# Performance work log

Hardware: AMD Instinct MI355X
Metric: run time of the kernel (lower is better)

The kernel has to match this reference:

```python
import jax, jax.numpy as jnp
import numpy as np

B, S, E, D, H, DH, FF, L = 8, 1024, 256, 1024, 16, 64, 4096, 12
TIME_DIM = 4096
MAX_PERIOD = 10000.0


def setup_inputs() -> dict:
    key = jax.random.key(0)
    ks = jax.random.split(key, 12)
    n = lambda k, shp: jax.random.normal(k, shp, dtype=jnp.float32) * 0.02
    return dict(
        inputs=jax.random.normal(ks[0], (B, S, 2 * E), dtype=jnp.float32),
        time=jax.random.uniform(ks[1], (B,), dtype=jnp.float32),
        in_W=n(ks[2], (2 * E, D)), in_b=jnp.zeros((D,), jnp.float32),
        out_W=n(ks[3], (D, E)), out_b=jnp.zeros((E,), jnp.float32),
        t_W1=n(ks[4], (D, TIME_DIM)), t_b1=jnp.zeros((TIME_DIM,), jnp.float32),
        t_W2=n(ks[5], (TIME_DIM, D)), t_b2=jnp.zeros((D,), jnp.float32),
        ln_scale=jnp.ones((L, D), jnp.float32),
        ln_bias=jnp.zeros((L, D), jnp.float32),
        proj_W=n(ks[6], (L, D, 3 * H * DH + 2 * FF)),
        attn_W=n(ks[7], (L, H * DH, D)),
        ff_W=n(ks[8], (L, FF, D)),
    )


def _layernorm(x, g, b):
    m = jnp.mean(x, axis=-1, keepdims=True)
    v = jnp.mean(jnp.square(x - m), axis=-1, keepdims=True)
    return (x - m) * jax.lax.rsqrt(v + 1e-5) * g + b


def reference(inputs, time, in_W, in_b, out_W, out_b, t_W1, t_b1, t_W2, t_b2,
              ln_scale, ln_bias, proj_W, attn_W, ff_W):
    # --- time embedding (SinusoidalTimeEmbedding -> Linear -> GELU -> Linear -> GELU) ---
    half = D // 2
    inv_ts = jnp.exp(jnp.arange(half, dtype=jnp.float32) * (-np.log(MAX_PERIOD) / (half - 1.0)))
    ts = time[:, None] * inv_ts[None, :]                      # [B, D/2]
    temb = jnp.concatenate([jnp.sin(ts), jnp.cos(ts)], -1)     # [B, D]
    temb = jax.nn.gelu(temb @ t_W1 + t_b1, approximate=False)
    temb = jax.nn.gelu(temb @ t_W2 + t_b2, approximate=False)  # [B, D]
    # --- fixed position embedding ---
    inv_freq = 1.0 / (MAX_PERIOD ** (jnp.arange(0, D, 2, dtype=jnp.float32) / D))
    sinu = jnp.arange(S, dtype=jnp.float32)[:, None] * inv_freq[None, :]  # [S, D/2]
    pos = jnp.concatenate([jnp.sin(sinu), jnp.cos(sinu)], -1)             # [S, D]
    # --- input projection + additive embeddings ---
    h = inputs @ in_W + in_b + pos[None] + temb[:, None, :]    # [B, S, D]
    scale = 1.0 / np.sqrt(DH)

    def block(h, params):
        g, bln, Wp, Wa, Wf = params
        u = _layernorm(h, g, bln)
        proj = u @ Wp                                          # [B, S, 3*H*DH + 2*FF]
        q, k, v, ff, gate = jnp.split(
            proj, [H * DH, 2 * H * DH, 3 * H * DH, 3 * H * DH + FF], axis=-1)
        q = q.reshape(B, S, H, DH).transpose(0, 2, 1, 3)       # [B, H, S, DH]
        k = k.reshape(B, S, H, DH).transpose(0, 2, 1, 3)
        v = v.reshape(B, S, H, DH).transpose(0, 2, 1, 3)
        score = jnp.einsum('bhsd,bhtd->bhst', q, k) * scale
        w = jax.nn.softmax(score, axis=-1)
        a = jnp.einsum('bhst,bhtd->bhsd', w, v)
        a = a.transpose(0, 2, 1, 3).reshape(B, S, H * DH)      # merge heads
        attn_out = a @ Wa
        ff_out = (ff * jax.nn.gelu(gate, approximate=True)) @ Wf  # tanh GELU per torch
        return h + attn_out + ff_out, None

    h, _ = jax.lax.scan(block, h, (ln_scale, ln_bias, proj_W, attn_W, ff_W))
    return h @ out_W + out_b
```

## Files before the change

### kernel.cpp

```cpp
#include <hip/hip_runtime.h>
#include <hip/hip_bf16.h>
#include <math.h>

static constexpr int B_ = 8, S_ = 1024, E_ = 256, D_ = 1024, H_ = 16, DH_ = 64,
                     FF_ = 4096, L_ = 12, TDIM_ = 4096;
static constexpr int BS_ = B_ * S_;
static constexpr int PROJN_ = 3 * H_ * DH_ + 2 * FF_;
static constexpr int PROJ3_ = 3 * H_ * DH_;
static constexpr int AOW_ = H_ * DH_ + FF_;

typedef __attribute__((ext_vector_type(8))) short bf16x8;
typedef __attribute__((ext_vector_type(4))) short bf16x4;
typedef __attribute__((ext_vector_type(4))) float f32x4;

__device__ __forceinline__ float b2f(short b) {
    return __uint_as_float(((unsigned)(unsigned short)b) << 16);
}
__device__ __forceinline__ short f2b(float f) {
    __hip_bfloat16 h = __float2bfloat16(f);
    return *reinterpret_cast<short*>(&h);
}
__device__ __forceinline__ float gelu_exact(float x) {
    return 0.5f * x * (1.f + erff(x * 0.70710678118654752440f));
}
__device__ __forceinline__ float gelu_tanh(float x) {
    float u2 = 1.59576912160573070f * (x + 0.044715f * x * x * x);
    return x / (1.f + __expf(-u2));
}

#define GLOAD16(g, l)                                                     \
    __builtin_amdgcn_global_load_lds(                                     \
        (const __attribute__((address_space(1))) void*)(g),               \
        (__attribute__((address_space(3))) void*)(l), 16, 0, 0)

__global__ void temb0_kernel(const float* __restrict__ time, float* __restrict__ temb0) {
    int b = blockIdx.x;
    int i = threadIdx.x;
    float inv_ts = expf((float)i * (-logf(10000.f) / 511.f));
    float ts = time[b] * inv_ts;
    temb0[b * D_ + i] = sinf(ts);
    temb0[b * D_ + 512 + i] = cosf(ts);
}

__global__ void pos_kernel(float* __restrict__ pos) {
    int s = blockIdx.x;
    int j = threadIdx.x;
    float inv_freq = expf((float)j * (-logf(10000.f) / 512.f));
    float arg = (float)s * inv_freq;
    pos[s * D_ + j] = sinf(arg);
    pos[s * D_ + 512 + j] = cosf(arg);
}

__global__ void tmlp_kernel(const float* __restrict__ A, const float* __restrict__ Bw,
                            const float* __restrict__ bias, float* __restrict__ C,
                            int K, int N) {
    __shared__ float Ast[8][256];
    __shared__ float red2[16][16][9];
    int t = threadIdx.x;
    int col = t & 15, ks = t >> 4;
    int n = blockIdx.x * 16 + col;
    float acc[8];
#pragma unroll
    for (int b = 0; b < 8; ++b) acc[b] = 0.f;
    for (int c0 = 0; c0 < K; c0 += 256) {
#pragma unroll
        for (int i = 0; i < 8; ++i) {
            int idx = t + i * 256;
            Ast[idx >> 8][idx & 255] = A[(idx >> 8) * K + c0 + (idx & 255)];
        }
        __syncthreads();
#pragma unroll
        for (int i = 0; i < 16; ++i) {
            int k = ks * 16 + i;
            float w = Bw[(size_t)(c0 + k) * N + n];
#pragma unroll
            for (int b = 0; b < 8; ++b) acc[b] = fmaf(Ast[b][k], w, acc[b]);
        }
        __syncthreads();
    }
#pragma unroll
    for (int b = 0; b < 8; ++b) red2[ks][col][b] = acc[b];
    __syncthreads();
    if (t < 128) {
        int c2 = t >> 3, b = t & 7;
        float s = 0.f;
#pragma unroll
        for (int k2 = 0; k2 < 16; ++k2) s += red2[k2][c2][b];
        int nn = blockIdx.x * 16 + c2;
        C[(size_t)b * N + nn] = gelu_exact(s + bias[nn]);
    }
}

__global__ void addpe_kernel(float* __restrict__ h, const float* __restrict__ pos,
                             const float* __restrict__ temb) {
    size_t idx = (size_t)blockIdx.x * 256 + threadIdx.x;
    int d = (int)(idx & 1023);
    int s = (int)((idx >> 10) & 1023);
    int b = (int)(idx >> 20);
    h[idx] += pos[s * D_ + d] + temb[b * D_ + d];
}

__global__ void f2b4_kernel(const float* __restrict__ in, __hip_bfloat16* __restrict__ out) {
    size_t i = ((size_t)blockIdx.x * 256 + threadIdx.x) * 4;
    float4 v = *reinterpret_cast<const float4*>(in + i);
    bf16x4 o;
    o[0] = f2b(v.x); o[1] = f2b(v.y); o[2] = f2b(v.z); o[3] = f2b(v.w);
    *reinterpret_cast<bf16x4*>(reinterpret_cast<short*>(out) + i) = o;
}

template <int PERM>
__global__ void convT_kernel(const float* __restrict__ W, __hip_bfloat16* __restrict__ Wt,
                             int K, int N, int outStride, int colOff) {
    __shared__ float tile[64][65];
    int t = threadIdx.x;
    int n0 = blockIdx.x * 64, k0 = blockIdx.y * 64;
#pragma unroll
    for (int i = 0; i < 4; ++i) {
        int idx = t + i * 256;
        int row = idx >> 4, c4 = (idx & 15) * 4;
        float4 v = *reinterpret_cast<const float4*>(W + (size_t)(k0 + row) * N + n0 + c4);
        tile[row][c4 + 0] = v.x; tile[row][c4 + 1] = v.y;
        tile[row][c4 + 2] = v.z; tile[row][c4 + 3] = v.w;
    }
    __syncthreads();
#pragma unroll
    for (int i = 0; i < 4; ++i) {
        int idx = t + i * 256;
        int n = idx >> 4, k4 = (idx & 15) * 4;
        int ng = n0 + n;
        size_t orow;
        if (PERM) {
            if (ng < 3072) orow = ng;
            else if (ng < 7168) { int j = ng - 3072; orow = 3072 + (j >> 7) * 256 + (j & 127); }
            else { int j = ng - 7168; orow = 3072 + (j >> 7) * 256 + 128 + (j & 127); }
        } else {
            orow = ng;
        }
        bf16x4 o;
#pragma unroll
        for (int j = 0; j < 4; ++j) o[j] = f2b(tile[k4 + j][n]);
        *reinterpret_cast<bf16x4*>(reinterpret_cast<short*>(Wt) + orow * outStride + colOff + k0 + k4) = o;
    }
}

__global__ void ln_kernel(const float* __restrict__ h, const float* __restrict__ g,
                          const float* __restrict__ bb, __hip_bfloat16* __restrict__ u) {
    int row = blockIdx.x;
    int t = threadIdx.x;
    const float4 v = reinterpret_cast<const float4*>(h + (size_t)row * D_)[t];
    __shared__ float red[8];
    float s = v.x + v.y + v.z + v.w;
    for (int m8 = 1; m8 < 64; m8 <<= 1) s += __shfl_xor(s, m8, 64);
    if ((t & 63) == 0) red[t >> 6] = s;
    __syncthreads();
    float mean = (red[0] + red[1] + red[2] + red[3]) * (1.f / 1024.f);
    float dx = v.x - mean, dy = v.y - mean, dz = v.z - mean, dw = v.w - mean;
    float sq = dx * dx + dy * dy + dz * dz + dw * dw;
    for (int m8 = 1; m8 < 64; m8 <<= 1) sq += __shfl_xor(sq, m8, 64);
    if ((t & 63) == 0) red[4 + (t >> 6)] = sq;
    __syncthreads();
    float var = (red[4] + red[5] + red[6] + red[7]) * (1.f / 1024.f);
    float inv = rsqrtf(var + 1e-5f);
    int c = t * 4;
    bf16x4 o;
    o[0] = f2b(dx * inv * g[c + 0] + bb[c + 0]);
    o[1] = f2b(dy * inv * g[c + 1] + bb[c + 1]);
    o[2] = f2b(dz * inv * g[c + 2] + bb[c + 2]);
    o[3] = f2b(dw * inv * g[c + 3] + bb[c + 3]);
    *reinterpret_cast<bf16x4*>(reinterpret_cast<short*>(u) + (size_t)row * D_ + c) = o;
}

template <int MODE, int BIAS>
__global__ __launch_bounds__(256) void mfma_gemm(
    const __hip_bfloat16* __restrict__ A, const __hip_bfloat16* __restrict__ Bt,
    const float* __restrict__ bias, float* __restrict__ Cf,
    __hip_bfloat16* __restrict__ Cb, int M, int N, int K) {
    __shared__ __align__(16) char As[128 * 64];
    __shared__ __align__(16) char Bs[128 * 64];
    int t = threadIdx.x;
    int lane = t & 63, wid = t >> 6;
    int m0 = blockIdx.y * 128, n0 = blockIdx.x * 128;
    size_t rowb = (size_t)K * 2;
    int srow = wid * 32 + (lane >> 2);
    int scol = (lane & 3) * 16;
    const char* ag0 = (const char*)A + (size_t)(m0 + srow) * rowb + scol;
    const char* ag1 = (const char*)A + (size_t)(m0 + srow + 16) * rowb + scol;
    const char* bg0 = (const char*)Bt + (size_t)(n0 + srow) * rowb + scol;
    const char* bg1 = (const char*)Bt + (size_t)(n0 + srow + 16) * rowb + scol;
    int lb0 = wid * 32 * 64;
    int lb1 = lb0 + 16 * 64;
    int wr = (wid >> 1) * 64, wc = (wid & 1) * 64;
    int lr = lane & 15;
    int a_base = (wr + lr) * 64 + (lane >> 4) * 16;
    int b_base = (wc + lr) * 64 + (lane >> 4) * 16;
    f32x4 acc[4][4] = {};
    int nkt = K >> 5;
    for (int kt = 0; kt < nkt; ++kt) {
        GLOAD16(ag0, As + lb0);
        GLOAD16(ag1, As + lb1);
        GLOAD16(bg0, Bs + lb0);
        GLOAD16(bg1, Bs + lb1);
        ag0 += 64; ag1 += 64; bg0 += 64; bg1 += 64;
        __syncthreads();
        bf16x8 af[4], bf[4];
#pragma unroll
        for (int f = 0; f < 4; ++f) {
            af[f] = *reinterpret_cast<const bf16x8*>(As + a_base + f * 1024);
            bf[f] = *reinterpret_cast<const bf16x8*>(Bs + b_base + f * 1024);
        }
        __builtin_amdgcn_s_setprio(1);
#pragma unroll
        for (int i = 0; i < 4; ++i)
#pragma unroll
            for (int j = 0; j < 4; ++j)
                acc[i][j] = __builtin_amdgcn_mfma_f32_16x16x32_bf16(af[i], bf[j], acc[i][j], 0, 0, 0);
        __builtin_amdgcn_s_setprio(0);
        __syncthreads();
    }
    int crow0 = m0 + wr + (lane >> 4) * 4;
    int ccol0 = n0 + wc + lr;
#pragma unroll
    for (int i = 0; i < 4; ++i) {
#pragma unroll
        for (int j = 0; j < 4; ++j) {
            int col = ccol0 + j * 16;
            float bv = BIAS ? bias[col] : 0.f;
            f32x4 v = acc[i][j];
#pragma unroll
            for (int r = 0; r < 4; ++r) {
                size_t o = (size_t)(crow0 + i * 16 + r) * N + col;
                float val = v[r] + bv;
                if (MODE == 0) Cf[o] = val;
                else if (MODE == 1) Cb[o] = __float2bfloat16(val);
                else Cf[o] += val;
            }
        }
    }
}

template <int MODE>
__global__ __launch_bounds__(512, 2) void gemm256(
    const __hip_bfloat16* __restrict__ A, const __hip_bfloat16* __restrict__ Bt,
    float* __restrict__ Cf, __hip_bfloat16* __restrict__ Cb,
    __hip_bfloat16* __restrict__ Fb, int M, int N, int K) {
    __shared__ __align__(16) char lds[131072];
    const int t = threadIdx.x;
    const int lane = t & 63, wid = t >> 6;
    const int lr = lane & 15, g = lane >> 4;
    const int wr = wid >> 2, wc = wid & 3;
    const int m0 = blockIdx.y * 256, n0 = blockIdx.x * 256;
    const size_t rowb = (size_t)K * 2;
    const int NT = K >> 6;
    const int srow = lane >> 2;
    const int scol = ((lane & 3) ^ (((lane >> 5) & 1) << 1)) * 16;
    const int ga = (g ^ (((lr >> 3) & 1) << 1)) * 16;
    const int arow = wr * 16 + lr;
    const int brow = wc * 16 + lr;
    const char* Ab = (const char*)A;
    const char* Bb = (const char*)Bt;

    auto stage = [&](int mat, int kt, int hh) {
        if (kt >= NT) return;
        int rbase = (mat ? n0 : m0) + hh * 128 + wid * 16 + srow;
        const char* src = (mat ? Bb : Ab) + (size_t)rbase * rowb + (size_t)kt * 128 + scol;
        char* dst = lds + mat * 65536 + (kt & 1) * 32768 + (hh * 128 + wid * 16) * 64;
        GLOAD16(src, dst);
        GLOAD16(src + 64, dst + 16384);
    };

    f32x4 acc[8][4] = {};
    bf16x8 af[4][2], bfr[4][2];

    stage(0, 0, 0); stage(0, 0, 1); stage(1, 0, 0); stage(1, 0, 1);
    stage(0, 1, 0); stage(1, 1, 0); stage(1, 1, 1);
    asm volatile("s_waitcnt vmcnt(6)" ::: "memory");
    __builtin_amdgcn_s_barrier();

    for (int kt = 0; kt < NT; ++kt) {
        const int p = kt & 1;
        const char* la = lds + p * 32768;
        const char* lb = lds + 65536 + p * 32768;
#pragma unroll
        for (int mi = 0; mi < 4; ++mi)
#pragma unroll
            for (int kk = 0; kk < 2; ++kk)
                af[mi][kk] = *reinterpret_cast<const bf16x8*>(
                    la + kk * 16384 + (mi * 32 + arow) * 64 + ga);
#pragma unroll
        for (int n = 0; n < 2; ++n)
#pragma unroll
            for (int kk = 0; kk < 2; ++kk)
                bfr[n][kk] = *reinterpret_cast<const bf16x8*>(
                    lb + kk * 16384 + (n * 64 + brow) * 64 + ga);
        stage(0, kt + 1, 1);
        __builtin_amdgcn_s_barrier();
        asm volatile("s_waitcnt lgkmcnt(0)" ::: "memory");
        __builtin_amdgcn_sched_barrier(0);
        __builtin_amdgcn_s_setprio(1);
#pragma unroll
        for (int mi = 0; mi < 4; ++mi)
#pragma unroll
            for (int n = 0; n < 2; ++n)
#pragma unroll
                for (int kk = 0; kk < 2; ++kk)
                    acc[mi][n] = __builtin_amdgcn_mfma_f32_16x16x32_bf16(
                        af[mi][kk], bfr[n][kk], acc[mi][n], 0, 0, 0);
        __builtin_amdgcn_s_setprio(0);
        __builtin_amdgcn_s_barrier();
#pragma unroll
        for (int n = 2; n < 4; ++n)
#pragma unroll
            for (int kk = 0; kk < 2; ++kk)
                bfr[n][kk] = *reinterpret_cast<const bf16x8*>(
                    lb + kk * 16384 + (n * 64 + brow) * 64 + ga);
        stage(0, kt + 2, 0);
        __builtin_amdgcn_s_barrier();
        asm volatile("s_waitcnt lgkmcnt(0)" ::: "memory");
        __builtin_amdgcn_sched_barrier(0);
        __builtin_amdgcn_s_setprio(1);
#pragma unroll
        for (int mi = 0; mi < 4; ++mi)
#pragma unroll
            for (int n = 2; n < 4; ++n)
#pragma unroll
                for (int kk = 0; kk < 2; ++kk)
                    acc[mi][n] = __builtin_amdgcn_mfma_f32_16x16x32_bf16(
                        af[mi][kk], bfr[n][kk], acc[mi][n], 0, 0, 0);
        __builtin_amdgcn_s_setprio(0);
        __builtin_amdgcn_s_barrier();
#pragma unroll
        for (int mi = 0; mi < 4; ++mi)
#pragma unroll
            for (int kk = 0; kk < 2; ++kk)
                af[mi][kk] = *reinterpret_cast<const bf16x8*>(
                    la + kk * 16384 + ((mi + 4) * 32 + arow) * 64 + ga);
        stage(1, kt + 2, 0);
        __builtin_amdgcn_s_barrier();
        asm volatile("s_waitcnt lgkmcnt(0)" ::: "memory");
        __builtin_amdgcn_sched_barrier(0);
        __builtin_amdgcn_s_setprio(1);
#pragma unroll
        for (int mi = 0; mi < 4; ++mi)
#pragma unroll
            for (int n = 2; n < 4; ++n)
#pragma unroll
                for (int kk = 0; kk < 2; ++kk)
                    acc[mi + 4][n] = __builtin_amdgcn_mfma_f32_16x16x32_bf16(
                        af[mi][kk], bfr[n][kk], acc[mi + 4][n], 0, 0, 0);
        __builtin_amdgcn_s_setprio(0);
        __builtin_amdgcn_s_barrier();
        stage(1, kt + 2, 1);
        if (kt < NT - 2) {
            asm volatile("s_waitcnt vmcnt(6)" ::: "memory");
        } else {
            asm volatile("s_waitcnt vmcnt(0)" ::: "memory");
        }
        __builtin_amdgcn_s_barrier();
        __builtin_amdgcn_s_setprio(1);
#pragma unroll
        for (int mi = 0; mi < 4; ++mi)
#pragma unroll
            for (int n = 0; n < 2; ++n)
#pragma unroll
                for (int kk = 0; kk < 2; ++kk)
                    acc[mi + 4][n] = __builtin_amdgcn_mfma_f32_16x16x32_bf16(
                        af[mi][kk], bfr[n][kk], acc[mi + 4][n], 0, 0, 0);
        __builtin_amdgcn_s_setprio(0);
        __builtin_amdgcn_s_barrier();
    }
    if (MODE == 3 && blockIdx.x >= 12) {
        int jb = ((int)blockIdx.x - 12) * 128;
#pragma unroll
        for (int m = 0; m < 8; ++m) {
            int crow = m0 + m * 32 + wr * 16 + g * 4;
#pragma unroll
            for (int n = 0; n < 2; ++n) {
                int ffcol = jb + n * 64 + wc * 16 + lr;
                f32x4 fv = acc[m][n];
                f32x4 gv = acc[m][n + 2];
#pragma unroll
                for (int r = 0; r < 4; ++r) {
                    float val = fv[r] * gelu_tanh(gv[r]);
                    Fb[(size_t)(crow + r) * AOW_ + ffcol] = __float2bfloat16(val);
                }
            }
        }
        return;
    }
#pragma unroll
    for (int m = 0; m < 8; ++m) {
        int crow = m0 + m * 32 + wr * 16 + g * 4;
#pragma unroll
        for (int n = 0; n < 4; ++n) {
            int col = n0 + n * 64 + wc * 16 + lr;
            f32x4 v = acc[m][n];
#pragma unroll
            for (int r = 0; r < 4; ++r) {
                if (MODE == 3) Cb[(size_t)(crow + r) * PROJ3_ + col] = __float2bfloat16(v[r]);
                else if (MODE == 0) Cf[(size_t)(crow + r) * N + col] = v[r];
                else if (MODE == 1) Cb[(size_t)(crow + r) * N + col] = __float2bfloat16(v[r]);
                else Cf[(size_t)(crow + r) * N + col] += v[r];
            }
        }
    }
}

__global__ __launch_bounds__(256, 2) void attn_kernel(
    const __hip_bfloat16* __restrict__ proj, __hip_bfloat16* __restrict__ ao) {
    __shared__ __align__(16) char ksm[64 * 128];
    __shared__ __align__(16) char vsm[64 * 128];
    __shared__ __align__(16) char psm[4 * 16 * 128];
    int wgid = blockIdx.x;
    int xcd = wgid & 7, slot = wgid >> 3;
    int group = xcd * 16 + (slot >> 4);
    int qt = slot & 15;
    int head = group & 15, b = group >> 4;
    int t = threadIdx.x;
    int lane = t & 63, w = t >> 6;
    int r = lane & 15, g = lane >> 4;
    int r7s = (r & 7) << 4;
    int q0 = qt * 64;
    int qcol = head * 64;
    const __hip_bfloat16* pb = proj + (size_t)b * S_ * PROJ3_;
    bf16x8 qf[2];
#pragma unroll
    for (int kk = 0; kk < 2; ++kk)
        qf[kk] = *reinterpret_cast<const bf16x8*>(
            pb + (size_t)(q0 + w * 16 + r) * PROJ3_ + qcol + kk * 32 + g * 8);
    int krow = lane >> 3;
    int kcolswz = ((lane & 7) ^ krow) * 8;
    int vdg = lane & 7;
    float m = -1e30f, l = 0.f;
    f32x4 o_acc[4] = {};
    char* pw = psm + w * 2048;
    for (int kt = 0; kt < 16; ++kt) {
        int k0 = kt * 64;
#pragma unroll
        for (int c = 0; c < 2; ++c) {
            const __hip_bfloat16* src =
                pb + (size_t)(k0 + w * 16 + c * 8 + krow) * PROJ3_ + 1024 + qcol + kcolswz;
            GLOAD16(src, ksm + (w * 16 + c * 8) * 128);
        }
#pragma unroll
        for (int it = 0; it < 2; ++it) {
            int kv = it * 32 + w * 8 + krow;
            bf16x8 vv = *reinterpret_cast<const bf16x8*>(
                pb + (size_t)(k0 + kv) * PROJ3_ + 2048 + qcol + vdg * 8);
            int kv2 = kv * 2;
#pragma unroll
            for (int i = 0; i < 8; ++i) {
                int j = (i + vdg) & 7;
                int d = vdg * 8 + j;
                *reinterpret_cast<short*>(vsm + d * 128 + (kv2 ^ ((d & 7) << 4))) = vv[j];
            }
        }
        __syncthreads();
        f32x4 st[4] = {};
        __builtin_amdgcn_s_setprio(1);
#pragma unroll
        for (int j = 0; j < 4; ++j) {
#pragma unroll
            for (int kk = 0; kk < 2; ++kk) {
                bf16x8 kf = *reinterpret_cast<const bf16x8*>(
                    ksm + (j * 16 + r) * 128 + ((((kk * 4 + g) << 4) ^ r7s)));
                st[j] = __builtin_amdgcn_mfma_f32_16x16x32_bf16(kf, qf[kk], st[j], 0, 0, 0);
            }
        }
        __builtin_amdgcn_s_setprio(0);
        float tmax = -1e30f;
#pragma unroll
        for (int j = 0; j < 4; ++j)
#pragma unroll
            for (int rr = 0; rr < 4; ++rr) {
                st[j][rr] *= 0.125f;
                tmax = fmaxf(tmax, st[j][rr]);
            }
        tmax = fmaxf(tmax, __shfl_xor(tmax, 16, 64));
        tmax = fmaxf(tmax, __shfl_xor(tmax, 32, 64));
        float mnew = fmaxf(m, tmax);
        float rsum = 0.f;
#pragma unroll
        for (int j = 0; j < 4; ++j)
#pragma unroll
            for (int rr = 0; rr < 4; ++rr) {
                float p = __expf(st[j][rr] - mnew);
                st[j][rr] = p;
                rsum += p;
            }
        rsum += __shfl_xor(rsum, 16, 64);
        rsum += __shfl_xor(rsum, 32, 64);
        float alpha = __expf(m - mnew);
        l = l * alpha + rsum;
        m = mnew;
#pragma unroll
        for (int j = 0; j < 4; ++j)
#pragma unroll
            for (int rr = 0; rr < 4; ++rr) {
                int kv2 = j * 32 + g * 8 + rr * 2;
                *reinterpret_cast<short*>(pw + r * 128 + (kv2 ^ r7s)) = f2b(st[j][rr]);
            }
        asm volatile("s_waitcnt lgkmcnt(0)" ::: "memory");
        __builtin_amdgcn_sched_barrier(0);
        float ar[4];
#pragma unroll
        for (int rr = 0; rr < 4; ++rr) ar[rr] = __shfl(alpha, g * 4 + rr, 64);
#pragma unroll
        for (int dt = 0; dt < 4; ++dt)
#pragma unroll
            for (int rr = 0; rr < 4; ++rr) o_acc[dt][rr] *= ar[rr];
        __builtin_amdgcn_s_setprio(1);
#pragma unroll
        for (int kk = 0; kk < 2; ++kk) {
            bf16x8 pf = *reinterpret_cast<const bf16x8*>(
                pw + r * 128 + ((((kk * 4 + g) << 4) ^ r7s)));
#pragma unroll
            for (int dt = 0; dt < 4; ++dt) {
                bf16x8 vf = *reinterpret_cast<const bf16x8*>(
                    vsm + (dt * 16 + r) * 128 + ((((kk * 4 + g) << 4) ^ r7s)));
                o_acc[dt] = __builtin_amdgcn_mfma_f32_16x16x32_bf16(pf, vf, o_acc[dt], 0, 0, 0);
            }
        }
        __builtin_amdgcn_s_setprio(0);
        __syncthreads();
    }
    float linv = 1.f / l;
    float lr4[4];
#pragma unroll
    for (int rr = 0; rr < 4; ++rr) lr4[rr] = __shfl(linv, g * 4 + rr, 64);
    short* ap = reinterpret_cast<short*>(ao);
#pragma unroll
    for (int dt = 0; dt < 4; ++dt)
#pragma unroll
        for (int rr = 0; rr < 4; ++rr) {
            size_t o = ((size_t)b * S_ + q0 + w * 16 + g * 4 + rr) * (size_t)AOW_ +
                       qcol + dt * 16 + r;
            ap[o] = f2b(o_acc[dt][rr] * lr4[rr]);
        }
}

extern "C" void kernel_launch(void* const* d_in, const int* in_sizes, int n_in,
                              void* d_out, int out_size, void* d_ws, size_t ws_size,
                              hipStream_t stream) {
    const float* inputs = (const float*)d_in[0];
    const float* time = (const float*)d_in[1];
    const float* in_W = (const float*)d_in[2];
    const float* in_b = (const float*)d_in[3];
    const float* out_W = (const float*)d_in[4];
    const float* out_b = (const float*)d_in[5];
    const float* t_W1 = (const float*)d_in[6];
    const float* t_b1 = (const float*)d_in[7];
    const float* t_W2 = (const float*)d_in[8];
    const float* t_b2 = (const float*)d_in[9];
    const float* ln_scale = (const float*)d_in[10];
    const float* ln_bias = (const float*)d_in[11];
    const float* proj_W = (const float*)d_in[12];
    const float* attn_W = (const float*)d_in[13];
    const float* ff_W = (const float*)d_in[14];
    float* out = (float*)d_out;

    float* ws = (float*)d_ws;
    size_t off = 0;
    float* temb0 = ws + off; off += 8 * 1024;
    float* tact = ws + off;  off += 8 * 4096;
    float* temb = ws + off;  off += 8 * 1024;
    float* pos = ws + off;   off += (size_t)S_ * D_;
    float* h = ws + off;     off += (size_t)BS_ * D_;
    __hip_bfloat16* u = (__hip_bfloat16*)(ws + off);      off += (size_t)BS_ * D_ / 2;
    __hip_bfloat16* proj = (__hip_bfloat16*)(ws + off);   off += (size_t)BS_ * PROJ3_ / 2;
    __hip_bfloat16* ao = (__hip_bfloat16*)(ws + off);     off += (size_t)BS_ * AOW_ / 2;
    __hip_bfloat16* hb = (__hip_bfloat16*)(ws + off);     off += (size_t)BS_ * D_ / 2;
    __hip_bfloat16* inbf = (__hip_bfloat16*)(ws + off);   off += (size_t)BS_ * (2 * E_) / 2;
    __hip_bfloat16* in_Wt = (__hip_bfloat16*)(ws + off);  off += (size_t)(2 * E_) * D_ / 2;
    __hip_bfloat16* out_Wt = (__hip_bfloat16*)(ws + off); off += (size_t)D_ * E_ / 2;
    __hip_bfloat16* Wpt = (__hip_bfloat16*)(ws + off);    off += (size_t)D_ * PROJN_ / 2;
    __hip_bfloat16* Waft = (__hip_bfloat16*)(ws + off);   off += (size_t)D_ * AOW_ / 2;

    dim3 blk(256);

    temb0_kernel<<<B_, 512, 0, stream>>>(time, temb0);
    tmlp_kernel<<<TDIM_ / 16, blk, 0, stream>>>(temb0, t_W1, t_b1, tact, D_, TDIM_);
    tmlp_kernel<<<D_ / 16, blk, 0, stream>>>(tact, t_W2, t_b2, temb, TDIM_, D_);
    pos_kernel<<<S_, 512, 0, stream>>>(pos);
    f2b4_kernel<<<(BS_ * 2 * E_) / 1024, blk, 0, stream>>>(inputs, inbf);
    convT_kernel<0><<<dim3(D_ / 64, (2 * E_) / 64), blk, 0, stream>>>(
        in_W, in_Wt, 2 * E_, D_, 2 * E_, 0);
    convT_kernel<0><<<dim3(E_ / 64, D_ / 64), blk, 0, stream>>>(
        out_W, out_Wt, D_, E_, D_, 0);
    mfma_gemm<0, 1><<<dim3(D_ / 128, BS_ / 128), blk, 0, stream>>>(
        inbf, in_Wt, in_b, h, nullptr, BS_, D_, 2 * E_);
    addpe_kernel<<<(BS_ * D_) / 256, blk, 0, stream>>>(h, pos, temb);

    for (int l = 0; l < L_; ++l) {
        const float* Wp = proj_W + (size_t)l * D_ * PROJN_;
        const float* Wa = attn_W + (size_t)l * (H_ * DH_) * D_;
        const float* Wf = ff_W + (size_t)l * FF_ * D_;
        convT_kernel<1><<<dim3(PROJN_ / 64, D_ / 64), blk, 0, stream>>>(
            Wp, Wpt, D_, PROJN_, D_, 0);
        convT_kernel<0><<<dim3(D_ / 64, D_ / 64), blk, 0, stream>>>(
            Wa, Waft, D_, D_, AOW_, 0);
        convT_kernel<0><<<dim3(D_ / 64, FF_ / 64), blk, 0, stream>>>(
            Wf, Waft, FF_, D_, AOW_, D_);
        ln_kernel<<<BS_, blk, 0, stream>>>(h, ln_scale + l * D_, ln_bias + l * D_, u);
        gemm256<3><<<dim3(PROJN_ / 256, BS_ / 256), dim3(512), 0, stream>>>(
            u, Wpt, nullptr, proj, ao + D_, BS_, PROJN_, D_);
        attn_kernel<<<dim3(2048), blk, 0, stream>>>(proj, ao);
        mfma_gemm<2, 0><<<dim3(D_ / 128, BS_ / 128), blk, 0, stream>>>(
            ao, Waft, nullptr, h, nullptr, BS_, D_, AOW_);
    }
    f2b4_kernel<<<(BS_ * D_) / 1024, blk, 0, stream>>>(h, hb);
    mfma_gemm<0, 1><<<dim3(E_ / 128, BS_ / 128), blk, 0, stream>>>(
        hb, out_Wt, out_b, out, nullptr, BS_, E_, D_);
}
```

Measured before the change: 5.589 ms.

## Write V transposed from projection GEMM, fuse weight converts, swizzle blocks, fuse PE add

The projection GEMM epilogue now writes V directly in a per-head transposed layout, so the attention kernel can load V tiles with direct 16-byte global-to-LDS loads instead of scattering shorts into LDS. The three per-layer weight convert/transpose launches become one combined launch. The gemm256 grid gets a block-index swizzle for better L2 locality, and the positional and time embedding add is folded into the input GEMM epilogue, removing a full pass over h. This costs strided 8-byte stores in the V epilogue and extra gathers in the input GEMM epilogue.

Result: faster. 5.392 ms (-3.5%).

```diff
diff --git a/kernel.cpp b/kernel.cpp
--- a/kernel.cpp
+++ b/kernel.cpp
@@ -6,7 +6,7 @@
                      FF_ = 4096, L_ = 12, TDIM_ = 4096;
 static constexpr int BS_ = B_ * S_;
 static constexpr int PROJN_ = 3 * H_ * DH_ + 2 * FF_;
-static constexpr int PROJ3_ = 3 * H_ * DH_;
+static constexpr int PROJK_ = 2 * H_ * DH_;
 static constexpr int AOW_ = H_ * DH_ + FF_;
 
 typedef __attribute__((ext_vector_type(8))) short bf16x8;
@@ -91,15 +91,6 @@
     }
 }
 
-__global__ void addpe_kernel(float* __restrict__ h, const float* __restrict__ pos,
-                             const float* __restrict__ temb) {
-    size_t idx = (size_t)blockIdx.x * 256 + threadIdx.x;
-    int d = (int)(idx & 1023);
-    int s = (int)((idx >> 10) & 1023);
-    int b = (int)(idx >> 20);
-    h[idx] += pos[s * D_ + d] + temb[b * D_ + d];
-}
-
 __global__ void f2b4_kernel(const float* __restrict__ in, __hip_bfloat16* __restrict__ out) {
     size_t i = ((size_t)blockIdx.x * 256 + threadIdx.x) * 4;
     float4 v = *reinterpret_cast<const float4*>(in + i);
@@ -108,12 +99,13 @@
     *reinterpret_cast<bf16x4*>(reinterpret_cast<short*>(out) + i) = o;
 }
 
-template <int PERM>
-__global__ void convT_kernel(const float* __restrict__ W, __hip_bfloat16* __restrict__ Wt,
-                             int K, int N, int outStride, int colOff) {
+__device__ __forceinline__ void convT_body(const float* __restrict__ W,
+                                           __hip_bfloat16* __restrict__ Wt,
+                                           int K, int N, int outStride, int colOff,
+                                           int perm, int bx, int by) {
     __shared__ float tile[64][65];
     int t = threadIdx.x;
-    int n0 = blockIdx.x * 64, k0 = blockIdx.y * 64;
+    int n0 = bx * 64, k0 = by * 64;
 #pragma unroll
     for (int i = 0; i < 4; ++i) {
         int idx = t + i * 256;
@@ -129,7 +121,7 @@
         int n = idx >> 4, k4 = (idx & 15) * 4;
         int ng = n0 + n;
         size_t orow;
-        if (PERM) {
+        if (perm) {
             if (ng < 3072) orow = ng;
             else if (ng < 7168) { int j = ng - 3072; orow = 3072 + (j >> 7) * 256 + (j & 127); }
             else { int j = ng - 7168; orow = 3072 + (j >> 7) * 256 + 128 + (j & 127); }
@@ -140,6 +132,26 @@
 #pragma unroll
         for (int j = 0; j < 4; ++j) o[j] = f2b(tile[k4 + j][n]);
         *reinterpret_cast<bf16x4*>(reinterpret_cast<short*>(Wt) + orow * outStride + colOff + k0 + k4) = o;
+    }
+}
+
+__global__ void convT_kernel(const float* __restrict__ W, __hip_bfloat16* __restrict__ Wt,
+                             int K, int N, int outStride, int colOff) {
+    convT_body(W, Wt, K, N, outStride, colOff, 0, blockIdx.x, blockIdx.y);
+}
+
+__global__ void convT3_kernel(const float* __restrict__ Wp, const float* __restrict__ Wa,
+                              const float* __restrict__ Wf, __hip_bfloat16* __restrict__ Wpt,
+                              __hip_bfloat16* __restrict__ Waft) {
+    int bid = blockIdx.x;
+    if (bid < 2816) {
+        convT_body(Wp, Wpt, D_, PROJN_, D_, 0, 1, bid % 176, bid / 176);
+    } else if (bid < 3072) {
+        int i2 = bid - 2816;
+        convT_body(Wa, Waft, D_, D_, AOW_, 0, 0, i2 & 15, i2 >> 4);
+    } else {
+        int i2 = bid - 3072;
+        convT_body(Wf, Waft, FF_, D_, AOW_, D_, 0, i2 & 15, i2 >> 4);
     }
 }
 
@@ -170,11 +182,12 @@
     *reinterpret_cast<bf16x4*>(reinterpret_cast<short*>(u) + (size_t)row * D_ + c) = o;
 }
 
-template <int MODE, int BIAS>
+template <int MODE, int BIAS, int ADDPE>
 __global__ __launch_bounds__(256) void mfma_gemm(
     const __hip_bfloat16* __restrict__ A, const __hip_bfloat16* __restrict__ Bt,
     const float* __restrict__ bias, float* __restrict__ Cf,
-    __hip_bfloat16* __restrict__ Cb, int M, int N, int K) {
+    __hip_bfloat16* __restrict__ Cb, const float* __restrict__ pe_pos,
+    const float* __restrict__ pe_temb, int M, int N, int K) {
     __shared__ __align__(16) char As[128 * 64];
     __shared__ __align__(16) char Bs[128 * 64];
     int t = threadIdx.x;
@@ -228,8 +241,12 @@
             f32x4 v = acc[i][j];
 #pragma unroll
             for (int r = 0; r < 4; ++r) {
-                size_t o = (size_t)(crow0 + i * 16 + r) * N + col;
+                int row = crow0 + i * 16 + r;
+                size_t o = (size_t)row * N + col;
                 float val = v[r] + bv;
+                if (ADDPE)
+                    val += pe_pos[(size_t)(row & 1023) * D_ + col] +
+                           pe_temb[(size_t)(row >> 10) * D_ + col];
                 if (MODE == 0) Cf[o] = val;
                 else if (MODE == 1) Cb[o] = __float2bfloat16(val);
                 else Cf[o] += val;
@@ -242,13 +259,19 @@
 __global__ __launch_bounds__(512, 2) void gemm256(
     const __hip_bfloat16* __restrict__ A, const __hip_bfloat16* __restrict__ Bt,
     float* __restrict__ Cf, __hip_bfloat16* __restrict__ Cb,
-    __hip_bfloat16* __restrict__ Fb, int M, int N, int K) {
+    __hip_bfloat16* __restrict__ Fb, __hip_bfloat16* __restrict__ Vt,
+    int M, int N, int K) {
     __shared__ __align__(16) char lds[131072];
     const int t = threadIdx.x;
     const int lane = t & 63, wid = t >> 6;
     const int lr = lane & 15, g = lane >> 4;
     const int wr = wid >> 2, wc = wid & 3;
-    const int m0 = blockIdx.y * 256, n0 = blockIdx.x * 256;
+    const int nbx = gridDim.x;
+    const int nwg = nbx * gridDim.y;
+    const int bid = blockIdx.y * nbx + blockIdx.x;
+    const int swz = (bid & 7) * (nwg >> 3) + (bid >> 3);
+    const int bx = swz % nbx, by = swz / nbx;
+    const int m0 = by * 256, n0 = bx * 256;
     const size_t rowb = (size_t)K * 2;
     const int NT = K >> 6;
     const int srow = lane >> 2;
@@ -368,8 +391,8 @@
         __builtin_amdgcn_s_setprio(0);
         __builtin_amdgcn_s_barrier();
     }
-    if (MODE == 3 && blockIdx.x >= 12) {
-        int jb = ((int)blockIdx.x - 12) * 128;
+    if (MODE == 3 && bx >= 12) {
+        int jb = (bx - 12) * 128;
 #pragma unroll
         for (int m = 0; m < 8; ++m) {
             int crow = m0 + m * 32 + wr * 16 + g * 4;
@@ -387,6 +410,26 @@
         }
         return;
     }
+    if (MODE == 3 && bx >= 8) {
+#pragma unroll
+        for (int m = 0; m < 8; ++m) {
+            int crow = m0 + m * 32 + wr * 16 + g * 4;
+            int b = crow >> 10, s = crow & 1023;
+#pragma unroll
+            for (int n = 0; n < 4; ++n) {
+                int col = n0 + n * 64 + wc * 16 + lr;
+                int head = (col - 2048) >> 6, d = col & 63;
+                f32x4 v = acc[m][n];
+                bf16x4 o;
+#pragma unroll
+                for (int r = 0; r < 4; ++r) o[r] = f2b(v[r]);
+                *reinterpret_cast<bf16x4*>(
+                    reinterpret_cast<short*>(Vt) +
+                    ((size_t)(b * 16 + head) * 64 + d) * 1024 + s) = o;
+            }
+        }
+        return;
+    }
 #pragma unroll
     for (int m = 0; m < 8; ++m) {
         int crow = m0 + m * 32 + wr * 16 + g * 4;
@@ -396,7 +439,7 @@
             f32x4 v = acc[m][n];
 #pragma unroll
             for (int r = 0; r < 4; ++r) {
-                if (MODE == 3) Cb[(size_t)(crow + r) * PROJ3_ + col] = __float2bfloat16(v[r]);
+                if (MODE == 3) Cb[(size_t)(crow + r) * PROJK_ + col] = __float2bfloat16(v[r]);
                 else if (MODE == 0) Cf[(size_t)(crow + r) * N + col] = v[r];
                 else if (MODE == 1) Cb[(size_t)(crow + r) * N + col] = __float2bfloat16(v[r]);
                 else Cf[(size_t)(crow + r) * N + col] += v[r];
@@ -406,7 +449,8 @@
 }
 
 __global__ __launch_bounds__(256, 2) void attn_kernel(
-    const __hip_bfloat16* __restrict__ proj, __hip_bfloat16* __restrict__ ao) {
+    const __hip_bfloat16* __restrict__ proj, const __hip_bfloat16* __restrict__ vt,
+    __hip_bfloat16* __restrict__ ao) {
     __shared__ __align__(16) char ksm[64 * 128];
     __shared__ __align__(16) char vsm[64 * 128];
     __shared__ __align__(16) char psm[4 * 16 * 128];
@@ -421,15 +465,15 @@
     int r7s = (r & 7) << 4;
     int q0 = qt * 64;
     int qcol = head * 64;
-    const __hip_bfloat16* pb = proj + (size_t)b * S_ * PROJ3_;
+    const __hip_bfloat16* pb = proj + (size_t)b * S_ * PROJK_;
+    const char* vtb = (const char*)(vt + ((size_t)(b * 16 + head) * 64) * 1024);
     bf16x8 qf[2];
 #pragma unroll
     for (int kk = 0; kk < 2; ++kk)
         qf[kk] = *reinterpret_cast<const bf16x8*>(
-            pb + (size_t)(q0 + w * 16 + r) * PROJ3_ + qcol + kk * 32 + g * 8);
-    int krow = lane >> 3;
-    int kcolswz = ((lane & 7) ^ krow) * 8;
-    int vdg = lane & 7;
+            pb + (size_t)(q0 + w * 16 + r) * PROJK_ + qcol + kk * 32 + g * 8);
+    int srow8 = lane >> 3;
+    int sgrp = lane & 7;
     float m = -1e30f, l = 0.f;
     f32x4 o_acc[4] = {};
     char* pw = psm + w * 2048;
@@ -437,22 +481,16 @@
         int k0 = kt * 64;
 #pragma unroll
         for (int c = 0; c < 2; ++c) {
+            int krow = w * 16 + c * 8 + srow8;
             const __hip_bfloat16* src =
-                pb + (size_t)(k0 + w * 16 + c * 8 + krow) * PROJ3_ + 1024 + qcol + kcolswz;
+                pb + (size_t)(k0 + krow) * PROJK_ + 1024 + qcol + ((sgrp ^ (krow & 7)) << 3);
             GLOAD16(src, ksm + (w * 16 + c * 8) * 128);
         }
 #pragma unroll
-        for (int it = 0; it < 2; ++it) {
-            int kv = it * 32 + w * 8 + krow;
-            bf16x8 vv = *reinterpret_cast<const bf16x8*>(
-                pb + (size_t)(k0 + kv) * PROJ3_ + 2048 + qcol + vdg * 8);
-            int kv2 = kv * 2;
-#pragma unroll
-            for (int i = 0; i < 8; ++i) {
-                int j = (i + vdg) & 7;
-                int d = vdg * 8 + j;
-                *reinterpret_cast<short*>(vsm + d * 128 + (kv2 ^ ((d & 7) << 4))) = vv[j];
-            }
+        for (int c = 0; c < 2; ++c) {
+            int drow = w * 16 + c * 8 + srow8;
+            const char* src = vtb + (size_t)drow * 2048 + k0 * 2 + ((sgrp ^ (drow & 7)) << 4);
+            GLOAD16(src, vsm + (w * 16 + c * 8) * 128);
         }
         __syncthreads();
         f32x4 st[4] = {};
@@ -566,7 +604,8 @@
     float* pos = ws + off;   off += (size_t)S_ * D_;
     float* h = ws + off;     off += (size_t)BS_ * D_;
     __hip_bfloat16* u = (__hip_bfloat16*)(ws + off);      off += (size_t)BS_ * D_ / 2;
-    __hip_bfloat16* proj = (__hip_bfloat16*)(ws + off);   off += (size_t)BS_ * PROJ3_ / 2;
+    __hip_bfloat16* proj = (__hip_bfloat16*)(ws + off);   off += (size_t)BS_ * PROJK_ / 2;
+    __hip_bfloat16* vt = (__hip_bfloat16*)(ws + off);     off += (size_t)BS_ * D_ / 2;
     __hip_bfloat16* ao = (__hip_bfloat16*)(ws + off);     off += (size_t)BS_ * AOW_ / 2;
     __hip_bfloat16* hb = (__hip_bfloat16*)(ws + off);     off += (size_t)BS_ * D_ / 2;
     __hip_bfloat16* inbf = (__hip_bfloat16*)(ws + off);   off += (size_t)BS_ * (2 * E_) / 2;
@@ -582,32 +621,26 @@
     tmlp_kernel<<<D_ / 16, blk, 0, stream>>>(tact, t_W2, t_b2, temb, TDIM_, D_);
     pos_kernel<<<S_, 512, 0, stream>>>(pos);
     f2b4_kernel<<<(BS_ * 2 * E_) / 1024, blk, 0, stream>>>(inputs, inbf);
-    convT_kernel<0><<<dim3(D_ / 64, (2 * E_) / 64), blk, 0, stream>>>(
+    convT_kernel<<<dim3(D_ / 64, (2 * E_) / 64), blk, 0, stream>>>(
         in_W, in_Wt, 2 * E_, D_, 2 * E_, 0);
-    convT_kernel<0><<<dim3(E_ / 64, D_ / 64), blk, 0, stream>>>(
+    convT_kernel<<<dim3(E_ / 64, D_ / 64), blk, 0, stream>>>(
         out_W, out_Wt, D_, E_, D_, 0);
-    mfma_gemm<0, 1><<<dim3(D_ / 128, BS_ / 128), blk, 0, stream>>>(
-        inbf, in_Wt, in_b, h, nullptr, BS_, D_, 2 * E_);
-    addpe_kernel<<<(BS_ * D_) / 256, blk, 0, stream>>>(h, pos, temb);
+    mfma_gemm<0, 1, 1><<<dim3(D_ / 128, BS_ / 128), blk, 0, stream>>>(
+        inbf, in_Wt, in_b, h, nullptr, pos, temb, BS_, D_, 2 * E_);
 
     for (int l = 0; l < L_; ++l) {
         const float* Wp = proj_W + (size_t)l * D_ * PROJN_;
         const float* Wa = attn_W + (size_t)l * (H_ * DH_) * D_;
         const float* Wf = ff_W + (size_t)l * FF_ * D_;
-        convT_kernel<1><<<dim3(PROJN_ / 64, D_ / 64), blk, 0, stream>>>(
-            Wp, Wpt, D_, PROJN_, D_, 0);
-        convT_kernel<0><<<dim3(D_ / 64, D_ / 64), blk, 0, stream>>>(
-            Wa, Waft, D_, D_, AOW_, 0);
-        convT_kernel<0><<<dim3(D_ / 64, FF_ / 64), blk, 0, stream>>>(
-            Wf, Waft, FF_, D_, AOW_, D_);
+        convT3_kernel<<<dim3(4096), blk, 0, stream>>>(Wp, Wa, Wf, Wpt, Waft);
         ln_kernel<<<BS_, blk, 0, stream>>>(h, ln_scale + l * D_, ln_bias + l * D_, u);
         gemm256<3><<<dim3(PROJN_ / 256, BS_ / 256), dim3(512), 0, stream>>>(
-            u, Wpt, nullptr, proj, ao + D_, BS_, PROJN_, D_);
-        attn_kernel<<<dim3(2048), blk, 0, stream>>>(proj, ao);
-        mfma_gemm<2, 0><<<dim3(D_ / 128, BS_ / 128), blk, 0, stream>>>(
-            ao, Waft, nullptr, h, nullptr, BS_, D_, AOW_);
+            u, Wpt, nullptr, proj, ao + D_, vt, BS_, PROJN_, D_);
+        attn_kernel<<<dim3(2048), blk, 0, stream>>>(proj, vt, ao);
+        mfma_gemm<2, 0, 0><<<dim3(D_ / 128, BS_ / 128), blk, 0, stream>>>(
+            ao, Waft, nullptr, h, nullptr, nullptr, nullptr, BS_, D_, AOW_);
     }
     f2b4_kernel<<<(BS_ * D_) / 1024, blk, 0, stream>>>(h, hb);
-    mfma_gemm<0, 1><<<dim3(E_ / 128, BS_ / 128), blk, 0, stream>>>(
-        hb, out_Wt, out_b, out, nullptr, BS_, E_, D_);
-}
+    mfma_gemm<0, 1, 0><<<dim3(E_ / 128, BS_ / 128), blk, 0, stream>>>(
+        hb, out_Wt, out_b, out, nullptr, nullptr, nullptr, BS_, E_, D_);
+}
```
